# Kernel tuning notes

Measured on AMD Instinct MI355X. Metric: run time of the kernel, lower is better.

Reference implementation:

```python
import jax, jax.numpy as jnp
import numpy as np

H = 32          # num_heads
D = 64          # kv_channels (head dim)
HID = 2048      # hidden_size
MAXPOS = 2048   # max_seq_length


def _rotary_table(num_pos, dim):
    # [num_pos, dim]: sin for first dim/2 cols, cos for last dim/2 cols
    inv_freq = 1.0 / (10000.0 ** (jnp.arange(0, dim, 2, dtype=jnp.float32) / dim))
    t = jnp.arange(num_pos, dtype=jnp.float32)[:, None] * inv_freq[None, :]
    return jnp.concatenate([jnp.sin(t), jnp.cos(t)], axis=1)


def _apply_rope(x, sin, cos):
    # x: [B,S,H,D]; sin,cos: [B,S,D/2]
    sin = jnp.concatenate([sin, sin], axis=-1)[:, :, None, :]  # [B,S,1,D]
    cos = jnp.concatenate([cos, cos], axis=-1)[:, :, None, :]
    half = x.shape[-1] // 2
    x1, x2 = x[..., :half], x[..., half:]
    rot = jnp.concatenate([-x2, x1], axis=-1)
    return x * cos + rot * sin


def setup_inputs() -> dict:
    key = jax.random.key(0)
    k1, k2, k3, k4 = jax.random.split(key, 4)
    B, S = 2, 2048
    hidden_states = jax.random.normal(k1, (B, S, HID), jnp.float32)
    attention_mask = jax.random.randint(k2, (B, 1, S, S), 0, 2).astype(bool)
    position_ids = jnp.broadcast_to(jnp.arange(S, dtype=jnp.int32)[None, :], (B, S))
    W_qkv = jax.random.normal(k3, (3 * H * D, HID), jnp.float32) * 0.02
    W_o = jax.random.normal(k4, (HID, H * D), jnp.float32) * 0.02
    return {"hidden_states": hidden_states, "attention_mask": attention_mask,
            "position_ids": position_ids, "W_qkv": W_qkv, "W_o": W_o}


def reference(hidden_states, attention_mask, position_ids, W_qkv, W_o):
    B, S, _ = hidden_states.shape
    # fused QKV projection (nn.Linear: x @ W.T, no bias)
    qkv = hidden_states @ W_qkv.T                       # [B,S,3*H*D]
    qkv = qkv.reshape(B, S, H, 3 * D)
    q, k, v = jnp.split(qkv, 3, axis=-1)                # each [B,S,H,D]
    sincos = _rotary_table(MAXPOS, D)[position_ids]     # [B,S,D]
    sin, cos = jnp.split(sincos, 2, axis=-1)            # [B,S,D/2] each
    q = _apply_rope(q, sin, cos)
    k = _apply_rope(k, sin, cos)
    scale = jnp.sqrt(jnp.float32(D))
    scores = jnp.einsum('bqhd,bkhd->bhqk', q, k) / scale   # [B,H,S,S]
    scores = jnp.where(attention_mask, jnp.float32(-10000.0), scores)
    weights = jax.nn.softmax(scores, axis=-1)
    attn = jnp.einsum('bhqk,bkhd->bqhd', weights, v)       # [B,S,H,D]
    attn = attn.reshape(B, S, H * D)
    return attn @ W_o.T                                    # [B,S,HID]
```

## Files before the change

kernel.cpp:

```cpp
#include <hip/hip_runtime.h>

#define B_   2
#define S_   2048
#define H_   32
#define D_   64
#define HID_ 2048

typedef unsigned short ushort_t;
typedef __attribute__((ext_vector_type(8))) short short8;
typedef __attribute__((ext_vector_type(4))) float floatx4;
typedef __attribute__((ext_vector_type(4))) unsigned short ushort4v;

typedef const __attribute__((address_space(1))) char* gas_ptr;
typedef __attribute__((address_space(3))) char* las_ptr;

__device__ __forceinline__ float bf2f(ushort_t u) {
    union { unsigned int i; float f; } v; v.i = ((unsigned int)u) << 16; return v.f;
}
__device__ __forceinline__ ushort_t f2bf(float f) {
    union { float f; unsigned int i; } v; v.f = f;
    unsigned int x = v.i;
    unsigned int r = x + 0x7fffu + ((x >> 16) & 1u);
    return (ushort_t)(r >> 16);
}

__global__ __launch_bounds__(256) void cast_f32_bf16(const float* __restrict__ in,
                                                     ushort_t* __restrict__ out,
                                                     int n8) {
    int i = blockIdx.x * 256 + threadIdx.x;
    if (i >= n8) return;
    const float4* p = (const float4*)(in + (size_t)i * 8);
    float4 a = p[0], b = p[1];
    short8 o;
    o[0] = (short)f2bf(a.x); o[1] = (short)f2bf(a.y);
    o[2] = (short)f2bf(a.z); o[3] = (short)f2bf(a.w);
    o[4] = (short)f2bf(b.x); o[5] = (short)f2bf(b.y);
    o[6] = (short)f2bf(b.z); o[7] = (short)f2bf(b.w);
    *(short8*)(out + (size_t)i * 8) = o;
}

__global__ __launch_bounds__(256) void mask_pack(const int* __restrict__ m,
                                                 unsigned long long* __restrict__ bits) {
    int idx = blockIdx.x * 256 + threadIdx.x;
    unsigned long long bal = __ballot(m[idx] != 0);
    if ((threadIdx.x & 63) == 0) bits[idx >> 6] = bal;
}

template <bool OF32>
__global__ __launch_bounds__(256) void gemm_bt(const ushort_t* __restrict__ A,
                                               const ushort_t* __restrict__ Bm,
                                               void* __restrict__ Cv,
                                               int M, int N, int K) {
    __shared__ ushort_t lA[128 * 32];
    __shared__ ushort_t lB[128 * 32];
    const int tid  = threadIdx.x;
    const int lane = tid & 63, wave = tid >> 6;
    const int quad = lane >> 4, l16 = lane & 15;
    const int wm = wave >> 1, wn = wave & 1;
    const int m0 = blockIdx.y * 128, n0 = blockIdx.x * 128;

    const int srow = tid >> 2;
    const int gseg = (tid & 3) ^ ((tid >> 3) & 3);
    const ushort_t* gA = A + (size_t)(m0 + srow) * K + gseg * 8;
    const ushort_t* gB = Bm + (size_t)(n0 + srow) * K + gseg * 8;

    const int fseg = quad ^ ((l16 >> 1) & 3);

    floatx4 acc[4][4];
#pragma unroll
    for (int i = 0; i < 4; i++)
#pragma unroll
        for (int j = 0; j < 4; j++) acc[i][j] = (floatx4){0.f, 0.f, 0.f, 0.f};

    for (int k0 = 0; k0 < K; k0 += 32) {
#pragma unroll
        for (int j = 0; j < 2; j++) {
            __builtin_amdgcn_global_load_lds(
                (gas_ptr)(gA + (size_t)j * 64 * K + k0),
                (las_ptr)(lA + j * 2048 + wave * 512), 16, 0, 0);
            __builtin_amdgcn_global_load_lds(
                (gas_ptr)(gB + (size_t)j * 64 * K + k0),
                (las_ptr)(lB + j * 2048 + wave * 512), 16, 0, 0);
        }
        __syncthreads();

        short8 aF[4], bF[4];
#pragma unroll
        for (int mi = 0; mi < 4; mi++)
            aF[mi] = *(const short8*)&lA[(wm * 64 + mi * 16 + l16) * 32 + fseg * 8];
#pragma unroll
        for (int ni = 0; ni < 4; ni++)
            bF[ni] = *(const short8*)&lB[(wn * 64 + ni * 16 + l16) * 32 + fseg * 8];
#pragma unroll
        for (int mi = 0; mi < 4; mi++)
#pragma unroll
            for (int ni = 0; ni < 4; ni++)
                acc[mi][ni] = __builtin_amdgcn_mfma_f32_16x16x32_bf16(aF[mi], bF[ni], acc[mi][ni], 0, 0, 0);
        __syncthreads();
    }

#pragma unroll
    for (int mi = 0; mi < 4; mi++)
#pragma unroll
        for (int ni = 0; ni < 4; ni++)
#pragma unroll
            for (int r = 0; r < 4; r++) {
                int row = m0 + wm * 64 + mi * 16 + quad * 4 + r;
                int col = n0 + wn * 64 + ni * 16 + l16;
                if (OF32) ((float*)Cv)[(size_t)row * N + col] = acc[mi][ni][r];
                else      ((ushort_t*)Cv)[(size_t)row * N + col] = f2bf(acc[mi][ni][r]);
            }
}

__global__ __launch_bounds__(256) void rope_qk(const ushort_t* __restrict__ qkv,
                                               const int* __restrict__ pos,
                                               ushort_t* __restrict__ qr,
                                               ushort_t* __restrict__ kr) {
    int idx = blockIdx.x * 256 + threadIdx.x;
    int d = idx & 63;
    int s = (idx >> 6) & 2047;
    int h = (idx >> 17) & 31;
    int b = idx >> 22;
    size_t qbase = ((size_t)(b * S_ + s)) * (3 * H_ * D_) + h * (3 * D_);
    int i  = d & 31;
    int d2 = d ^ 32;
    float x   = bf2f(qkv[qbase + d]);
    float xp  = bf2f(qkv[qbase + d2]);
    float kx  = bf2f(qkv[qbase + 64 + d]);
    float kxp = bf2f(qkv[qbase + 64 + d2]);
    int   p   = pos[b * S_ + s];
    float inv = 1.0f / powf(10000.0f, (float)(2 * i) / 64.0f);
    float t   = (float)p * inv;
    float c = cosf(t), sn = sinf(t);
    float rq = (d < 32) ? -xp : xp;
    float rk = (d < 32) ? -kxp : kxp;
    float qo = (x * c + rq * sn) * 0.125f;
    float ko = kx * c + rk * sn;
    size_t o = ((size_t)(b * H_ + h) * S_ + s) * D_ + d;
    qr[o] = f2bf(qo);
    kr[o] = f2bf(ko);
}

__global__ __launch_bounds__(256) void v_trans(const ushort_t* __restrict__ qkv,
                                               ushort_t* __restrict__ vt) {
    int idx = blockIdx.x * 256 + threadIdx.x;
    int s = idx & 2047;
    int d = (idx >> 11) & 63;
    int h = (idx >> 17) & 31;
    int b = idx >> 22;
    vt[idx] = qkv[((size_t)(b * S_ + s)) * (3 * H_ * D_) + h * (3 * D_) + 128 + d];
}

__global__ __launch_bounds__(256) void attn_kernel(const ushort_t* __restrict__ qr,
                                                   const ushort_t* __restrict__ kr,
                                                   const ushort_t* __restrict__ vt,
                                                   const unsigned long long* __restrict__ mbits,
                                                   ushort_t* __restrict__ ctx) {
    __shared__ ushort_t lK[64 * 64];
    __shared__ ushort_t lV[64 * 64];
    __shared__ ushort_t lds_p[4][16][72];
    const int tid  = threadIdx.x;
    const int wave = tid >> 6, lane = tid & 63;
    const int quad = lane >> 4, l16 = lane & 15;

    const int id   = blockIdx.x;
    const int g    = (id & 7) | ((id >> 8) << 3);
    const int qblk = (id >> 3) & 31;
    const int b    = g >> 5;
    const int q0   = qblk * 64 + wave * 16;
    const size_t headBase = (size_t)g * S_ * D_;
    const unsigned long long* mrow = mbits + ((size_t)b * S_ + q0 + l16) * (S_ / 64);

    const int sr = lane >> 3, ss = lane & 7;
    const int gss = ss ^ sr;
    const ushort_t* gK0 = kr + headBase + (size_t)(wave * 16 + sr) * D_ + gss * 8;
    const ushort_t* gV0 = vt + headBase + (size_t)(wave * 16 + sr) * S_ + gss * 8;

    const int segA0 = ((quad)     ^ (l16 & 7)) * 8;
    const int segA1 = ((quad + 4) ^ (l16 & 7)) * 8;
    const int rowOff = (l16)*64;

    short8 qf0 = *(const short8*)(qr + headBase + (size_t)(q0 + l16) * D_ + quad * 8);
    short8 qf1 = *(const short8*)(qr + headBase + (size_t)(q0 + l16) * D_ + 32 + quad * 8);

    float l_st = 0.f;
    floatx4 o[4];
#pragma unroll
    for (int t = 0; t < 4; t++) o[t] = (floatx4){0.f, 0.f, 0.f, 0.f};

    for (int k0 = 0; k0 < S_; k0 += 64) {
#pragma unroll
        for (int i = 0; i < 2; i++) {
            __builtin_amdgcn_global_load_lds(
                (gas_ptr)(gK0 + (size_t)(k0 + i * 8) * D_),
                (las_ptr)(lK + (wave * 16 + i * 8) * 64), 16, 0, 0);
            __builtin_amdgcn_global_load_lds(
                (gas_ptr)(gV0 + (size_t)(i * 8) * S_ + k0),
                (las_ptr)(lV + (wave * 16 + i * 8) * 64), 16, 0, 0);
        }
        unsigned long long mb = mrow[k0 >> 6];
        __syncthreads();

        floatx4 scT[4];
#pragma unroll
        for (int t = 0; t < 4; t++) scT[t] = (floatx4){0.f, 0.f, 0.f, 0.f};
#pragma unroll
        for (int t = 0; t < 4; t++) {
            short8 kf0 = *(const short8*)&lK[t * 1024 + rowOff + segA0];
            short8 kf1 = *(const short8*)&lK[t * 1024 + rowOff + segA1];
            scT[t] = __builtin_amdgcn_mfma_f32_16x16x32_bf16(kf0, qf0, scT[t], 0, 0, 0);
            scT[t] = __builtin_amdgcn_mfma_f32_16x16x32_bf16(kf1, qf1, scT[t], 0, 0, 0);
        }

        float pv[4][4];
        float rs = 0.f;
#pragma unroll
        for (int t = 0; t < 4; t++)
#pragma unroll
            for (int r = 0; r < 4; r++) {
                int kl = t * 16 + quad * 4 + r;
                float e = __expf(scT[t][r]);
                e = ((mb >> kl) & 1ull) ? 0.f : e;
                pv[t][r] = e;
                rs += e;
            }
        l_st += rs;

#pragma unroll
        for (int t = 0; t < 4; t++) {
            ushort4v w;
            w[0] = f2bf(pv[t][0]); w[1] = f2bf(pv[t][1]);
            w[2] = f2bf(pv[t][2]); w[3] = f2bf(pv[t][3]);
            *(ushort4v*)&lds_p[wave][l16][t * 16 + quad * 4] = w;
        }
        short8 pf0 = *(const short8*)&lds_p[wave][l16][quad * 8];
        short8 pf1 = *(const short8*)&lds_p[wave][l16][32 + quad * 8];

#pragma unroll
        for (int t = 0; t < 4; t++) {
            short8 vf0 = *(const short8*)&lV[t * 1024 + rowOff + segA0];
            short8 vf1 = *(const short8*)&lV[t * 1024 + rowOff + segA1];
            o[t] = __builtin_amdgcn_mfma_f32_16x16x32_bf16(pf0, vf0, o[t], 0, 0, 0);
            o[t] = __builtin_amdgcn_mfma_f32_16x16x32_bf16(pf1, vf1, o[t], 0, 0, 0);
        }
        __syncthreads();
    }

    l_st += __shfl_xor(l_st, 16);
    l_st += __shfl_xor(l_st, 32);
    float li[4];
#pragma unroll
    for (int r = 0; r < 4; r++) li[r] = 1.0f / __shfl(l_st, quad * 4 + r, 16);
#pragma unroll
    for (int t = 0; t < 4; t++)
#pragma unroll
        for (int r = 0; r < 4; r++) {
            int srow = q0 + quad * 4 + r;
            ctx[((size_t)(b * S_) + srow) * (H_ * D_) + (g & 31) * D_ + t * 16 + l16] = f2bf(o[t][r] * li[r]);
        }
}

extern "C" void kernel_launch(void* const* d_in, const int* in_sizes, int n_in,
                              void* d_out, int out_size, void* d_ws, size_t ws_size,
                              hipStream_t stream) {
    const float* hidden          = (const float*)d_in[0];
    const int* mask              = (const int*)d_in[1];
    const int* pos               = (const int*)d_in[2];
    const float* Wqkv            = (const float*)d_in[3];
    const float* Wo              = (const float*)d_in[4];
    float* out                   = (float*)d_out;

    char* ws = (char*)d_ws;
    ushort_t* qkv     = (ushort_t*)(ws);
    ushort_t* ctx     = (ushort_t*)(ws);
    unsigned long long* mbits = (unsigned long long*)(ws + 16777216);
    ushort_t* Wo_bf   = (ushort_t*)(ws + 50331648);
    ushort_t* hid_bf  = (ushort_t*)(ws + 58720256);
    ushort_t* Wqkv_bf = (ushort_t*)(ws + 75497472);
    ushort_t* q_r     = (ushort_t*)(ws + 58720256);
    ushort_t* k_r     = (ushort_t*)(ws + 75497472);
    ushort_t* v_t     = (ushort_t*)(ws + 92274688);

    {
        int n8 = (B_ * S_ * HID_) / 8;
        cast_f32_bf16<<<n8 / 256, 256, 0, stream>>>(hidden, hid_bf, n8);
        n8 = (3 * H_ * D_ * HID_) / 8;
        cast_f32_bf16<<<n8 / 256, 256, 0, stream>>>(Wqkv, Wqkv_bf, n8);
        n8 = (HID_ * H_ * D_) / 8;
        cast_f32_bf16<<<n8 / 256, 256, 0, stream>>>(Wo, Wo_bf, n8);
    }

    gemm_bt<false><<<dim3((3 * H_ * D_) / 128, (B_ * S_) / 128), 256, 0, stream>>>(
        hid_bf, Wqkv_bf, qkv, B_ * S_, 3 * H_ * D_, HID_);

    int nElem = B_ * H_ * S_ * D_;
    rope_qk<<<nElem / 256, 256, 0, stream>>>(qkv, pos, q_r, k_r);
    v_trans<<<nElem / 256, 256, 0, stream>>>(qkv, v_t);

    mask_pack<<<(B_ * S_ * S_) / 256, 256, 0, stream>>>(mask, mbits);

    attn_kernel<<<2048, 256, 0, stream>>>(q_r, k_r, v_t, mbits, ctx);

    gemm_bt<true><<<dim3(HID_ / 128, (B_ * S_) / 128), 256, 0, stream>>>(
        ctx, Wo_bf, out, B_ * S_, HID_, H_ * D_);
}
```

Before: 430.4 us.

## Use hardware bf16 pack, exp2 softmax, 32-bit mask bits, and tiled V transpose

Replaces the software bf16 rounding with the v_cvt_pk_bf16_f32 instruction in the cast and attention kernels. It folds log2(e) into the Q scale so the softmax can call the native exp2 instead of __expf, and it splits the 64-bit mask test into 32-bit shifts. The V transpose now goes through an LDS tile with 16-byte vector loads and stores instead of a strided element-by-element gather. The rope inverse frequency uses exp2 in place of powf. This is several unrelated micro-optimisations at once, and the rounding of the new pack instruction may differ slightly on edge cases.

```diff
diff --git a/kernel.cpp b/kernel.cpp
--- a/kernel.cpp
+++ b/kernel.cpp
@@ -9,7 +9,6 @@
 typedef unsigned short ushort_t;
 typedef __attribute__((ext_vector_type(8))) short short8;
 typedef __attribute__((ext_vector_type(4))) float floatx4;
-typedef __attribute__((ext_vector_type(4))) unsigned short ushort4v;
 
 typedef const __attribute__((address_space(1))) char* gas_ptr;
 typedef __attribute__((address_space(3))) char* las_ptr;
@@ -22,6 +21,20 @@
     unsigned int x = v.i;
     unsigned int r = x + 0x7fffu + ((x >> 16) & 1u);
     return (ushort_t)(r >> 16);
+}
+
+__device__ __forceinline__ float fexp2(float x) {
+#if __has_builtin(__builtin_amdgcn_exp2f)
+    return __builtin_amdgcn_exp2f(x);
+#else
+    float r; asm("v_exp_f32 %0, %1" : "=v"(r) : "v"(x)); return r;
+#endif
+}
+
+__device__ __forceinline__ unsigned cvt_pk_bf16(float a, float b) {
+    unsigned r;
+    asm("v_cvt_pk_bf16_f32 %0, %1, %2" : "=v"(r) : "v"(a), "v"(b));
+    return r;
 }
 
 __global__ __launch_bounds__(256) void cast_f32_bf16(const float* __restrict__ in,
@@ -31,12 +44,12 @@
     if (i >= n8) return;
     const float4* p = (const float4*)(in + (size_t)i * 8);
     float4 a = p[0], b = p[1];
-    short8 o;
-    o[0] = (short)f2bf(a.x); o[1] = (short)f2bf(a.y);
-    o[2] = (short)f2bf(a.z); o[3] = (short)f2bf(a.w);
-    o[4] = (short)f2bf(b.x); o[5] = (short)f2bf(b.y);
-    o[6] = (short)f2bf(b.z); o[7] = (short)f2bf(b.w);
-    *(short8*)(out + (size_t)i * 8) = o;
+    uint4 o;
+    o.x = cvt_pk_bf16(a.x, a.y);
+    o.y = cvt_pk_bf16(a.z, a.w);
+    o.z = cvt_pk_bf16(b.x, b.y);
+    o.w = cvt_pk_bf16(b.z, b.w);
+    *(uint4*)(out + (size_t)i * 8) = o;
 }
 
 __global__ __launch_bounds__(256) void mask_pack(const int* __restrict__ m,
@@ -129,12 +142,12 @@
     float kx  = bf2f(qkv[qbase + 64 + d]);
     float kxp = bf2f(qkv[qbase + 64 + d2]);
     int   p   = pos[b * S_ + s];
-    float inv = 1.0f / powf(10000.0f, (float)(2 * i) / 64.0f);
+    float inv = fexp2((float)i * -0.41524101186092985f);
     float t   = (float)p * inv;
     float c = cosf(t), sn = sinf(t);
     float rq = (d < 32) ? -xp : xp;
     float rk = (d < 32) ? -kxp : kxp;
-    float qo = (x * c + rq * sn) * 0.125f;
+    float qo = (x * c + rq * sn) * 0.18033688011112042f;
     float ko = kx * c + rk * sn;
     size_t o = ((size_t)(b * H_ + h) * S_ + s) * D_ + d;
     qr[o] = f2bf(qo);
@@ -143,12 +156,27 @@
 
 __global__ __launch_bounds__(256) void v_trans(const ushort_t* __restrict__ qkv,
                                                ushort_t* __restrict__ vt) {
-    int idx = blockIdx.x * 256 + threadIdx.x;
-    int s = idx & 2047;
-    int d = (idx >> 11) & 63;
-    int h = (idx >> 17) & 31;
-    int b = idx >> 22;
-    vt[idx] = qkv[((size_t)(b * S_ + s)) * (3 * H_ * D_) + h * (3 * D_) + 128 + d];
+    __shared__ ushort_t tile[64][72];
+    const int bid = blockIdx.x;
+    const int g  = bid >> 5;
+    const int s0 = (bid & 31) * 64;
+    const int b = g >> 5, h = g & 31;
+    const int tid = threadIdx.x;
+    const int r = tid >> 2, c = (tid & 3) * 16;
+    const ushort_t* src = qkv + ((size_t)(b * S_) + s0 + r) * (3 * H_ * D_) + h * (3 * D_) + 128 + c;
+    *(short8*)&tile[r][c]     = *(const short8*)src;
+    *(short8*)&tile[r][c + 8] = *(const short8*)(src + 8);
+    __syncthreads();
+    const int d = tid >> 2, cs = (tid & 3) * 16;
+    ushort_t* dst = vt + ((size_t)g * D_ + d) * S_ + s0 + cs;
+    short8 o0, o1;
+#pragma unroll
+    for (int j = 0; j < 8; j++) {
+        o0[j] = (short)tile[cs + j][d];
+        o1[j] = (short)tile[cs + 8 + j][d];
+    }
+    *(short8*)dst       = o0;
+    *(short8*)(dst + 8) = o1;
 }
 
 __global__ __launch_bounds__(256) void attn_kernel(const ushort_t* __restrict__ qr,
@@ -212,26 +240,30 @@
             scT[t] = __builtin_amdgcn_mfma_f32_16x16x32_bf16(kf1, qf1, scT[t], 0, 0, 0);
         }
 
+        unsigned mlo = (unsigned)(mb >> (quad * 4));
+        unsigned mhi = (unsigned)(mb >> (quad * 4 + 32));
         float pv[4][4];
         float rs = 0.f;
 #pragma unroll
-        for (int t = 0; t < 4; t++)
+        for (int t = 0; t < 4; t++) {
+            unsigned msrc = (t < 2) ? mlo : mhi;
 #pragma unroll
             for (int r = 0; r < 4; r++) {
-                int kl = t * 16 + quad * 4 + r;
-                float e = __expf(scT[t][r]);
-                e = ((mb >> kl) & 1ull) ? 0.f : e;
+                int bitpos = (t & 1) * 16 + r;
+                float e = fexp2(scT[t][r]);
+                e = ((msrc >> bitpos) & 1u) ? 0.f : e;
                 pv[t][r] = e;
                 rs += e;
             }
+        }
         l_st += rs;
 
 #pragma unroll
         for (int t = 0; t < 4; t++) {
-            ushort4v w;
-            w[0] = f2bf(pv[t][0]); w[1] = f2bf(pv[t][1]);
-            w[2] = f2bf(pv[t][2]); w[3] = f2bf(pv[t][3]);
-            *(ushort4v*)&lds_p[wave][l16][t * 16 + quad * 4] = w;
+            uint2 w;
+            w.x = cvt_pk_bf16(pv[t][0], pv[t][1]);
+            w.y = cvt_pk_bf16(pv[t][2], pv[t][3]);
+            *(uint2*)&lds_p[wave][l16][t * 16 + quad * 4] = w;
         }
         short8 pf0 = *(const short8*)&lds_p[wave][l16][quad * 8];
         short8 pf1 = *(const short8*)&lds_p[wave][l16][32 + quad * 8];
@@ -295,7 +327,7 @@
 
     int nElem = B_ * H_ * S_ * D_;
     rope_qk<<<nElem / 256, 256, 0, stream>>>(qkv, pos, q_r, k_r);
-    v_trans<<<nElem / 256, 256, 0, stream>>>(qkv, v_t);
+    v_trans<<<B_ * H_ * (S_ / 64), 256, 0, stream>>>(qkv, v_t);
 
     mask_pack<<<(B_ * S_ * S_) / 256, 256, 0, stream>>>(mask, mbits);
 
```

Result: faster. 360.5 us (-16.2%).
